# Performance work log

Measured on AMD Instinct MI355X. Metric: run time of the kernel, lower is better.

The kernel has to match this reference:

```python
import jax, jax.numpy as jnp
import numpy as np
from jax import lax

P, T, A = 4096, 128, 32
K = int(P * 0.1)          # elite count = 409
TEMP, MOM, MIN_STD = 0.5, 0.1, 0.05
INF = jnp.float32(1e30)   # large finite stand-in for +inf (grad-safe)


def setup_inputs() -> dict:
    key = jax.random.key(0)
    k1, k2 = jax.random.split(key)
    obs_diffs = jax.random.uniform(k1, (P, T, T), dtype=jnp.float32)  # pairwise MSE costs >= 0
    means = jnp.zeros((T, 1, A), dtype=jnp.float32)
    stds = jnp.ones((T, 1, A), dtype=jnp.float32)
    noise = jax.random.normal(k2, (T, P, A), dtype=jnp.float32)
    return {"obs_diffs": obs_diffs, "means": means, "stds": stds, "noise": noise}


def _dtw_dists(obs_diffs):
    """DTW-style min-plus DP: D[i+1,j+1] = min(D[i,j+1], D[i+1,j], D[i,j]) + c[i,j].
    obs_diffs: [P, T, T] -> dists: [P] (= D[:, T, T])."""
    p = obs_diffs.shape[0]
    inf_col = jnp.full((p,), INF, dtype=obs_diffs.dtype)
    # row 0 of the (T+1)x(T+1) table: [0, inf, inf, ...]
    row0 = jnp.concatenate([jnp.zeros((p, 1), obs_diffs.dtype),
                            jnp.full((p, obs_diffs.shape[1]), INF, obs_diffs.dtype)], axis=1)

    def row_step(prev_row, c_row):  # prev_row [P, T+1], c_row [P, T]
        def inner(carry, xs):        # carry = new[j] (left neighbor), vectorized over P
            p_j1, p_j, c = xs        # prev[j+1], prev[j], cost  -- each [P]
            new = jnp.minimum(jnp.minimum(p_j1, p_j), carry) + c
            return new, new
        xs = (prev_row[:, 1:].T, prev_row[:, :-1].T, c_row.T)  # each [T, P]
        _, vals = lax.scan(inner, inf_col, xs)                  # vals [T, P]
        new_row = jnp.concatenate([inf_col[:, None], vals.T], axis=1)
        return new_row, None

    final_row, _ = lax.scan(row_step, row0, jnp.swapaxes(obs_diffs, 0, 1))
    return final_row[:, -1]


def reference(obs_diffs, means, stds, noise):
    # sample population of action trajectories
    actions = jnp.clip(means + stds * noise, -1.0, 1.0)        # [T, P, A]
    dists = _dtw_dists(obs_diffs)                               # [P]
    neg_top, idxs = lax.top_k(-dists, K)                        # K smallest dists
    elite_diffs = -neg_top                                      # [K]
    elite_actions = actions[:, idxs]                            # [T, K, A]
    min_diff = elite_diffs.min()
    score = jnp.exp(TEMP * (min_diff - elite_diffs))
    score = score / score.sum()
    ssum = score.sum()                                          # == 1, kept to match torch
    w = score[None, :, None]                                    # [1, K, 1]
    _mean = jnp.sum(w * elite_actions, axis=1, keepdims=True) / (ssum + 1e-9)   # [T,1,A]
    _std = jnp.sqrt(jnp.sum(w * (elite_actions - _mean) ** 2, axis=1, keepdims=True) / (ssum + 1e-9))
    _std = jnp.clip(_std, MIN_STD, 1.0)
    means_new = MOM * means + (1.0 - MOM) * _mean
    return jnp.stack([means_new, _std])                         # [2, T, 1, A]
```

## Files before the change

### kernel.cpp

```cpp
#include <hip/hip_runtime.h>
#include <math.h>

#define P_N 4096
#define T_N 128
#define A_N 32
#define K_N 409
#define TEMP_C 0.5f
#define MOM_C 0.1f
#define MIN_STD_C 0.05f
#define INF_F 1e30f

#define DPPMOV(dst, src, ctrl, oldv)                                          \
  {                                                                           \
    union { float f; int i; } _a, _b, _r;                                     \
    _a.f = (src); _b.f = (oldv);                                              \
    _r.i = __builtin_amdgcn_update_dpp(_b.i, _a.i, (ctrl), 0xF, 0xF, false);  \
    (dst) = _r.f;                                                             \
  }

__global__ __launch_bounds__(256) void dtw_kernel(const float* __restrict__ obs,
                                                  float* __restrict__ dists) {
  const int tid  = threadIdx.x;
  const int wave = tid >> 6;
  const int lane = tid & 63;
  const int half = lane >> 5;
  const int l    = lane & 31;
  const int p    = blockIdx.x * 8 + wave * 2 + half;
  const bool is0 = (l == 0);

  const float4* row = (const float4*)(obs + (size_t)p * (T_N * T_N)) + l;

  float P1 = INF_F, P2 = INF_F, P3 = INF_F, P4 = INF_F;
  float p0 = is0 ? 0.0f : INF_F;

  float4 cb0 = row[0];
  float4 cb1 = row[32];
  float4 cb2 = row[64];

  for (int r = 0; r < T_N; ++r) {
    float4 c = cb0;
    cb0 = cb1; cb1 = cb2;
    int rn = r + 3; if (rn > T_N - 1) rn = T_N - 1;
    cb2 = row[rn * 32];

    float a1 = fminf(P1, p0);
    float a2 = fminf(P2, P1);
    float a3 = fminf(P3, P2);
    float a4 = fminf(P4, P3);

    float B = a1 + c.x;
    B = fminf(B + c.y, a2 + c.y);
    B = fminf(B + c.z, a3 + c.z);
    B = fminf(B + c.w, a4 + c.w);
    float C = (c.x + c.y) + (c.z + c.w);

    float Bp, Cp;
    DPPMOV(Bp, B, 0x111, INF_F); DPPMOV(Cp, C, 0x111, 0.0f);
    B = fminf(Bp + C, B); C = Cp + C;
    DPPMOV(Bp, B, 0x112, INF_F); DPPMOV(Cp, C, 0x112, 0.0f);
    B = fminf(Bp + C, B); C = Cp + C;
    DPPMOV(Bp, B, 0x114, INF_F); DPPMOV(Cp, C, 0x114, 0.0f);
    B = fminf(Bp + C, B); C = Cp + C;
    DPPMOV(Bp, B, 0x118, INF_F); DPPMOV(Cp, C, 0x118, 0.0f);
    B = fminf(Bp + C, B); C = Cp + C;
    DPPMOV(Bp, B, 0x142, INF_F); DPPMOV(Cp, C, 0x142, 0.0f);
    B = fminf(Bp + C, B); C = Cp + C;

    float x;
    DPPMOV(x, B, 0x138, INF_F);
    x = is0 ? INF_F : x;

    float n1 = fminf(a1, x)  + c.x;
    float n2 = fminf(a2, n1) + c.y;
    float n3 = fminf(a3, n2) + c.z;
    float n4 = fminf(a4, n3) + c.w;

    p0 = x; P1 = n1; P2 = n2; P3 = n3; P4 = n4;
  }

  if (l == 31) dists[p] = P4;
}

__global__ __launch_bounds__(1024) void select_kernel(const float* __restrict__ dists,
                                                      int* __restrict__ elite_idx,
                                                      float* __restrict__ elite_wn,
                                                      float* __restrict__ meta) {
  __shared__ unsigned int skey[P_N];
  __shared__ __align__(16) unsigned int hist[256];
  __shared__ float elite_d[K_N];
  __shared__ int eqbuf[256];
  __shared__ float red[1024];
  __shared__ unsigned int sc_prefix, sc_minkey;
  __shared__ int sc_r, sc_cntlt, sc_cnteq;

  const int tid = threadIdx.x;

  unsigned int localmin = 0xFFFFFFFFu;
  for (int p = tid; p < P_N; p += 1024) {
    unsigned int k = __float_as_uint(dists[p]);
    skey[p] = k;
    if (k < localmin) localmin = k;
  }
  #pragma unroll
  for (int d = 32; d > 0; d >>= 1) {
    unsigned int o = __shfl_xor(localmin, (unsigned)d, 64);
    if (o < localmin) localmin = o;
  }
  if (tid == 0) { sc_minkey = 0xFFFFFFFFu; sc_cntlt = 0; sc_cnteq = 0;
                  sc_prefix = 0; sc_r = K_N - 1; }
  __syncthreads();
  if ((tid & 63) == 0) atomicMin(&sc_minkey, localmin);
  __syncthreads();

  unsigned int mask = 0;
  for (int shift = 24; shift >= 0; shift -= 8) {
    for (int b = tid; b < 256; b += 1024) hist[b] = 0;
    __syncthreads();
    unsigned int pref = sc_prefix;
    for (int p = tid; p < P_N; p += 1024) {
      unsigned int k = skey[p];
      if ((k & mask) == pref) atomicAdd(&hist[(k >> shift) & 255u], 1u);
    }
    __syncthreads();
    if (tid < 64) {
      unsigned h0 = hist[tid * 4 + 0], h1 = hist[tid * 4 + 1];
      unsigned h2 = hist[tid * 4 + 2], h3 = hist[tid * 4 + 3];
      unsigned s1 = h0 + h1, s2 = s1 + h2, s3 = s2 + h3;
      unsigned tot = s3;
      #pragma unroll
      for (int d = 1; d < 64; d <<= 1) {
        unsigned o = __shfl_up(tot, (unsigned)d, 64);
        if (tid >= d) tot += o;
      }
      unsigned base = tot - s3;
      unsigned rr = (unsigned)sc_r;
      if (rr >= base && rr < base + s3) {
        int bsel; unsigned lo;
        if (rr < base + h0)      { bsel = 0; lo = base; }
        else if (rr < base + s1) { bsel = 1; lo = base + h0; }
        else if (rr < base + s2) { bsel = 2; lo = base + s1; }
        else                     { bsel = 3; lo = base + s2; }
        sc_prefix |= (unsigned)(tid * 4 + bsel) << shift;
        sc_r = (int)(rr - lo);
      }
    }
    mask |= 0xFFu << shift;
    __syncthreads();
  }

  const unsigned int tk = sc_prefix;
  const int needeq = sc_r + 1;

  for (int p = tid; p < P_N; p += 1024) {
    unsigned int k = skey[p];
    if (k < tk) {
      int pos = atomicAdd(&sc_cntlt, 1);
      elite_idx[pos] = p;
      elite_d[pos]   = __uint_as_float(k);
    } else if (k == tk) {
      int ep = atomicAdd(&sc_cnteq, 1);
      if (ep < 256) eqbuf[ep] = p;
    }
  }
  __syncthreads();
  if (tid == 0) {
    int cl = sc_cntlt;
    int ce = sc_cnteq; if (ce > 256) ce = 256;
    for (int rsel = 0; rsel < needeq; ++rsel) {
      int best = 0x7FFFFFFF, bi = 0;
      for (int m = 0; m < ce; ++m) {
        int v = eqbuf[m];
        if (v < best) { best = v; bi = m; }
      }
      eqbuf[bi] = 0x7FFFFFFF;
      elite_idx[cl + rsel] = best;
      elite_d[cl + rsel]   = __uint_as_float(tk);
    }
  }
  __syncthreads();

  const float minf = __uint_as_float(sc_minkey);
  float s = 0.0f;
  if (tid < K_N) s = expf(TEMP_C * (minf - elite_d[tid]));
  red[tid] = s;
  for (int d = 512; d > 0; d >>= 1) {
    __syncthreads();
    if (tid < d) red[tid] += red[tid + d];
  }
  __syncthreads();
  const float S = red[0];
  __syncthreads();
  const float wn = (tid < K_N) ? (s / S) : 0.0f;
  red[tid] = wn;
  for (int d = 512; d > 0; d >>= 1) {
    __syncthreads();
    if (tid < d) red[tid] += red[tid + d];
  }
  __syncthreads();
  if (tid < K_N) elite_wn[tid] = wn;
  if (tid == 0) meta[0] = red[0];
}

__global__ __launch_bounds__(256) void elite_stats_kernel(
    const float* __restrict__ noise, const float* __restrict__ means,
    const float* __restrict__ stds, const int* __restrict__ elite_idx,
    const float* __restrict__ elite_wn, const float* __restrict__ meta,
    float* __restrict__ out) {
  const int t = blockIdx.x;
  const int tid = threadIdx.x;
  const int a  = tid & 31;
  const int er = tid >> 5;
  __shared__ int   sidx[K_N];
  __shared__ float swn[K_N];
  __shared__ float sM[8][32];
  __shared__ float sQ[8][32];

  for (int e = tid; e < K_N; e += 256) { sidx[e] = elite_idx[e]; swn[e] = elite_wn[e]; }
  __syncthreads();

  const float mn = means[t * A_N + a];
  const float sd = stds[t * A_N + a];
  const float* nrow = noise + (size_t)t * P_N * A_N;

  float M = 0.0f, Q = 0.0f;
  for (int e = er; e < K_N; e += 8) {
    const int idx = sidx[e];
    const float w = swn[e];
    float x = mn + sd * nrow[idx * A_N + a];
    x = fminf(1.0f, fmaxf(-1.0f, x));
    M += w * x;
    Q += w * x * x;
  }
  sM[er][a] = M; sQ[er][a] = Q;
  __syncthreads();

  if (tid < 32) {
    float Ms = 0.0f, Qs = 0.0f;
    #pragma unroll
    for (int r = 0; r < 8; ++r) { Ms += sM[r][a]; Qs += sQ[r][a]; }
    const float ssum = meta[0];
    const float D = ssum + 1e-9f;
    const float mu = Ms / D;
    float var = (Qs - 2.0f * mu * Ms + mu * mu * ssum) / D;
    float stdv = sqrtf(fmaxf(var, 0.0f));
    stdv = fminf(1.0f, fmaxf(MIN_STD_C, stdv));
    out[t * A_N + a]              = MOM_C * mn + (1.0f - MOM_C) * mu;
    out[T_N * A_N + t * A_N + a]  = stdv;
  }
}

extern "C" void kernel_launch(void* const* d_in, const int* in_sizes, int n_in,
                              void* d_out, int out_size, void* d_ws, size_t ws_size,
                              hipStream_t stream) {
  const float* obs   = (const float*)d_in[0];
  const float* means = (const float*)d_in[1];
  const float* stds  = (const float*)d_in[2];
  const float* noise = (const float*)d_in[3];
  float* out = (float*)d_out;

  float* dists     = (float*)d_ws;
  int*   elite_idx = (int*)(dists + P_N);
  float* elite_wn  = (float*)(elite_idx + 512);
  float* meta      = elite_wn + 512;

  dtw_kernel<<<P_N / 8, 256, 0, stream>>>(obs, dists);
  select_kernel<<<1, 1024, 0, stream>>>(dists, elite_idx, elite_wn, meta);
  elite_stats_kernel<<<T_N, 256, 0, stream>>>(noise, means, stds,
                                              elite_idx, elite_wn, meta, out);
}
```

Measured before the change: 448.3 us.

## Deepen DTW prefetch with nontemporal loads and streamline selection and stats kernels

The DTW kernel now prefetches four rows ahead instead of three and uses nontemporal vector loads for the cost matrix, which is read only once. The selection kernel gains per-wave histograms to cut LDS atomic contention, ballot-based compaction in place of per-thread atomics, and shuffle-based reductions in place of the shared-memory tree. The elite stats kernel doubles its block size to 512 threads. Together these aim to raise memory throughput in the dominant DTW stage and trim latency in the serial single-block stage, at the cost of an extra live register vector and more shared memory.

```diff
diff --git a/kernel.cpp b/kernel.cpp
--- a/kernel.cpp
+++ b/kernel.cpp
@@ -9,6 +9,8 @@
 #define MOM_C 0.1f
 #define MIN_STD_C 0.05f
 #define INF_F 1e30f
+
+typedef float vfloat4 __attribute__((ext_vector_type(4)));
 
 #define DPPMOV(dst, src, ctrl, oldv)                                          \
   {                                                                           \
@@ -28,20 +30,21 @@
   const int p    = blockIdx.x * 8 + wave * 2 + half;
   const bool is0 = (l == 0);
 
-  const float4* row = (const float4*)(obs + (size_t)p * (T_N * T_N)) + l;
+  const vfloat4* row = (const vfloat4*)(obs + (size_t)p * (T_N * T_N)) + l;
 
   float P1 = INF_F, P2 = INF_F, P3 = INF_F, P4 = INF_F;
   float p0 = is0 ? 0.0f : INF_F;
 
-  float4 cb0 = row[0];
-  float4 cb1 = row[32];
-  float4 cb2 = row[64];
+  vfloat4 cb0 = __builtin_nontemporal_load(row);
+  vfloat4 cb1 = __builtin_nontemporal_load(row + 32);
+  vfloat4 cb2 = __builtin_nontemporal_load(row + 64);
+  vfloat4 cb3 = __builtin_nontemporal_load(row + 96);
 
   for (int r = 0; r < T_N; ++r) {
-    float4 c = cb0;
-    cb0 = cb1; cb1 = cb2;
-    int rn = r + 3; if (rn > T_N - 1) rn = T_N - 1;
-    cb2 = row[rn * 32];
+    vfloat4 c = cb0;
+    cb0 = cb1; cb1 = cb2; cb2 = cb3;
+    int rn = r + 4; if (rn > T_N - 1) rn = T_N - 1;
+    cb3 = __builtin_nontemporal_load(row + rn * 32);
 
     float a1 = fminf(P1, p0);
     float a2 = fminf(P2, P1);
@@ -86,14 +89,17 @@
                                                       float* __restrict__ elite_wn,
                                                       float* __restrict__ meta) {
   __shared__ unsigned int skey[P_N];
-  __shared__ __align__(16) unsigned int hist[256];
+  __shared__ unsigned int histw[16 * 256];
   __shared__ float elite_d[K_N];
   __shared__ int eqbuf[256];
-  __shared__ float red[1024];
+  __shared__ float wsum[16];
   __shared__ unsigned int sc_prefix, sc_minkey;
   __shared__ int sc_r, sc_cntlt, sc_cnteq;
-
-  const int tid = threadIdx.x;
+  __shared__ float sS, sS2;
+
+  const int tid  = threadIdx.x;
+  const int wid  = tid >> 6;
+  const int lane = tid & 63;
 
   unsigned int localmin = 0xFFFFFFFFu;
   for (int p = tid; p < P_N; p += 1024) {
@@ -109,22 +115,30 @@
   if (tid == 0) { sc_minkey = 0xFFFFFFFFu; sc_cntlt = 0; sc_cnteq = 0;
                   sc_prefix = 0; sc_r = K_N - 1; }
   __syncthreads();
-  if ((tid & 63) == 0) atomicMin(&sc_minkey, localmin);
+  if (lane == 0) atomicMin(&sc_minkey, localmin);
   __syncthreads();
 
   unsigned int mask = 0;
   for (int shift = 24; shift >= 0; shift -= 8) {
-    for (int b = tid; b < 256; b += 1024) hist[b] = 0;
+    for (int b = tid; b < 16 * 256; b += 1024) histw[b] = 0;
     __syncthreads();
     unsigned int pref = sc_prefix;
     for (int p = tid; p < P_N; p += 1024) {
       unsigned int k = skey[p];
-      if ((k & mask) == pref) atomicAdd(&hist[(k >> shift) & 255u], 1u);
+      if ((k & mask) == pref)
+        atomicAdd(&histw[wid * 256 + ((k >> shift) & 255u)], 1u);
+    }
+    __syncthreads();
+    if (tid < 256) {
+      unsigned tot = 0;
+      #pragma unroll
+      for (int w = 0; w < 16; ++w) tot += histw[w * 256 + tid];
+      histw[tid] = tot;
     }
     __syncthreads();
     if (tid < 64) {
-      unsigned h0 = hist[tid * 4 + 0], h1 = hist[tid * 4 + 1];
-      unsigned h2 = hist[tid * 4 + 2], h3 = hist[tid * 4 + 3];
+      unsigned h0 = histw[tid * 4 + 0], h1 = histw[tid * 4 + 1];
+      unsigned h2 = histw[tid * 4 + 2], h3 = histw[tid * 4 + 3];
       unsigned s1 = h0 + h1, s2 = s1 + h2, s3 = s2 + h3;
       unsigned tot = s3;
       #pragma unroll
@@ -153,8 +167,13 @@
 
   for (int p = tid; p < P_N; p += 1024) {
     unsigned int k = skey[p];
-    if (k < tk) {
-      int pos = atomicAdd(&sc_cntlt, 1);
+    const bool lt = (k < tk);
+    unsigned long long m = __ballot(lt);
+    int base = 0;
+    if (lane == 0) base = atomicAdd(&sc_cntlt, (int)__popcll(m));
+    base = __shfl(base, 0, 64);
+    if (lt) {
+      int pos = base + (int)__popcll(m & ((1ull << lane) - 1ull));
       elite_idx[pos] = p;
       elite_d[pos]   = __uint_as_float(k);
     } else if (k == tk) {
@@ -180,28 +199,38 @@
   __syncthreads();
 
   const float minf = __uint_as_float(sc_minkey);
-  float s = 0.0f;
-  if (tid < K_N) s = expf(TEMP_C * (minf - elite_d[tid]));
-  red[tid] = s;
-  for (int d = 512; d > 0; d >>= 1) {
-    __syncthreads();
-    if (tid < d) red[tid] += red[tid + d];
-  }
-  __syncthreads();
-  const float S = red[0];
-  __syncthreads();
+  float s = (tid < K_N) ? expf(TEMP_C * (minf - elite_d[tid])) : 0.0f;
+  float t1 = s;
+  #pragma unroll
+  for (int d = 32; d > 0; d >>= 1) t1 += __shfl_xor(t1, (unsigned)d, 64);
+  if (lane == 0) wsum[wid] = t1;
+  __syncthreads();
+  if (tid == 0) {
+    float acc = 0.0f;
+    #pragma unroll
+    for (int w = 0; w < 16; ++w) acc += wsum[w];
+    sS = acc;
+  }
+  __syncthreads();
+  const float S = sS;
   const float wn = (tid < K_N) ? (s / S) : 0.0f;
-  red[tid] = wn;
-  for (int d = 512; d > 0; d >>= 1) {
-    __syncthreads();
-    if (tid < d) red[tid] += red[tid + d];
+  float t2 = wn;
+  #pragma unroll
+  for (int d = 32; d > 0; d >>= 1) t2 += __shfl_xor(t2, (unsigned)d, 64);
+  if (lane == 0) wsum[wid] = t2;
+  __syncthreads();
+  if (tid == 0) {
+    float acc = 0.0f;
+    #pragma unroll
+    for (int w = 0; w < 16; ++w) acc += wsum[w];
+    sS2 = acc;
   }
   __syncthreads();
   if (tid < K_N) elite_wn[tid] = wn;
-  if (tid == 0) meta[0] = red[0];
-}
-
-__global__ __launch_bounds__(256) void elite_stats_kernel(
+  if (tid == 0) meta[0] = sS2;
+}
+
+__global__ __launch_bounds__(512) void elite_stats_kernel(
     const float* __restrict__ noise, const float* __restrict__ means,
     const float* __restrict__ stds, const int* __restrict__ elite_idx,
     const float* __restrict__ elite_wn, const float* __restrict__ meta,
@@ -212,10 +241,10 @@
   const int er = tid >> 5;
   __shared__ int   sidx[K_N];
   __shared__ float swn[K_N];
-  __shared__ float sM[8][32];
-  __shared__ float sQ[8][32];
-
-  for (int e = tid; e < K_N; e += 256) { sidx[e] = elite_idx[e]; swn[e] = elite_wn[e]; }
+  __shared__ float sM[16][32];
+  __shared__ float sQ[16][32];
+
+  for (int e = tid; e < K_N; e += 512) { sidx[e] = elite_idx[e]; swn[e] = elite_wn[e]; }
   __syncthreads();
 
   const float mn = means[t * A_N + a];
@@ -223,7 +252,7 @@
   const float* nrow = noise + (size_t)t * P_N * A_N;
 
   float M = 0.0f, Q = 0.0f;
-  for (int e = er; e < K_N; e += 8) {
+  for (int e = er; e < K_N; e += 16) {
     const int idx = sidx[e];
     const float w = swn[e];
     float x = mn + sd * nrow[idx * A_N + a];
@@ -237,7 +266,7 @@
   if (tid < 32) {
     float Ms = 0.0f, Qs = 0.0f;
     #pragma unroll
-    for (int r = 0; r < 8; ++r) { Ms += sM[r][a]; Qs += sQ[r][a]; }
+    for (int r = 0; r < 16; ++r) { Ms += sM[r][a]; Qs += sQ[r][a]; }
     const float ssum = meta[0];
     const float D = ssum + 1e-9f;
     const float mu = Ms / D;
@@ -265,6 +294,6 @@
 
   dtw_kernel<<<P_N / 8, 256, 0, stream>>>(obs, dists);
   select_kernel<<<1, 1024, 0, stream>>>(dists, elite_idx, elite_wn, meta);
-  elite_stats_kernel<<<T_N, 256, 0, stream>>>(noise, means, stds,
+  elite_stats_kernel<<<T_N, 512, 0, stream>>>(noise, means, stds,
                                               elite_idx, elite_wn, meta, out);
 }
```

After: 429.6 us. 4.2% less time.
